# Performance work log

Hardware: AMD Instinct MI355X
Metric: run time of the kernel (lower is better)

The kernel has to match this reference:

```python
import jax, jax.numpy as jnp
import numpy as np

ACTIONS = 64
EMB = 32
DELTA = 16
EPS = 1e-5


def setup_inputs() -> dict:
    key = jax.random.key(0)
    k1, k2 = jax.random.split(key)
    n = 16384
    x = jax.random.normal(k1, (n, ACTIONS), dtype=jnp.float32)
    bn_weight = jnp.ones((ACTIONS,), dtype=jnp.float32)
    bn_bias = jnp.zeros((ACTIONS,), dtype=jnp.float32)
    emb_table = jax.random.normal(k2, ((2 * DELTA + 1) * ACTIONS, EMB), dtype=jnp.float32)
    return {"x": x, "bn_weight": bn_weight, "bn_bias": bn_bias, "emb_table": emb_table}


def reference(x, bn_weight, bn_bias, emb_table):
    n = x.shape[0]
    # BatchNorm1d in training mode: biased batch statistics over the batch dim
    mean = jnp.mean(x, axis=0)
    var = jnp.mean(jnp.square(x - mean), axis=0)
    xn = (x - mean) * jax.lax.rsqrt(var + EPS) * bn_weight + bn_bias
    t = jnp.clip(jnp.tanh(xn), -1.0 + 1e-5, 1.0 - 1e-5)  # [n, actions]

    ind_offset = jnp.arange(ACTIONS, dtype=jnp.int32)[None, :]  # [1, actions]
    xl = jnp.floor(t * DELTA)
    xli = ACTIONS * (xl.astype(jnp.int32) + DELTA) + ind_offset  # [n, actions]
    xl = xl / DELTA
    xh = jnp.floor(t * DELTA + 1.0)
    xhi = ACTIONS * (xh.astype(jnp.int32) + DELTA) + ind_offset
    xh = xh / DELTA

    bl = emb_table[xli]  # [n, actions, emb]
    bh = emb_table[xhi]  # [n, actions, emb]

    # h = bh/delta_inv*(t-xl) + bl/delta_inv*(xh-t), delta_inv = 1/DELTA
    t3 = t[..., None]
    h = bh * (DELTA * (t3 - xl[..., None])) + bl * (DELTA * (xh[..., None] - t3))
    return h
```

## Files before the change

### kernel.cpp

```cpp
#include <hip/hip_runtime.h>
#include <hip/hip_bf16.h>

#define ACTIONS 64
#define EMB 32
#define DELTA 16
#define EPS 1e-5f

typedef float f32x4 __attribute__((ext_vector_type(4)));

__device__ __forceinline__ float fast_tanhf(float x) {
    float e = __expf(2.0f * x);
    float r = __builtin_amdgcn_rcpf(1.0f + e);
    return 1.0f - 2.0f * r;
}

__global__ void __launch_bounds__(512) bn_stats_kernel(const f32x4* __restrict__ x4,
                                                       float* __restrict__ partial,
                                                       int total4 ) {
    const int tid = threadIdx.x;
    f32x4 s = {0.f, 0.f, 0.f, 0.f};
    f32x4 q = {0.f, 0.f, 0.f, 0.f};
    const int stride = gridDim.x * 512;
    for (int i = blockIdx.x * 512 + tid; i < total4; i += stride) {
        f32x4 v = x4[i];
        s += v;
        q += v * v;
    }
    __shared__ f32x4 ssum[512];
    __shared__ f32x4 ssq[512];
    ssum[tid] = s;
    ssq[tid] = q;
    __syncthreads();
    if (tid < 16) {
        f32x4 a = ssum[tid];
        f32x4 b = ssq[tid];
        #pragma unroll
        for (int k = 1; k < 32; ++k) {
            a += ssum[tid + 16 * k];
            b += ssq[tid + 16 * k];
        }
        float* ps = partial + blockIdx.x * 128;
        #pragma unroll
        for (int j = 0; j < 4; ++j) {
            ps[4 * tid + j]      = a[j];
            ps[64 + 4 * tid + j] = b[j];
        }
    }
}

__global__ void __launch_bounds__(256) spline_main_kernel(
        const f32x4* __restrict__ x4,
        const f32x4* __restrict__ emb4,
        const float* __restrict__ partial,
        const float* __restrict__ bn_w,
        const float* __restrict__ bn_b,
        f32x4* __restrict__ out4,
        float inv_n) {
    __shared__ f32x4 tab4[33 * 64];
    __shared__ f32x4 xs4[256];
    __shared__ float psum[2][8][16];

    const int tid     = threadIdx.x;
    const int colgrp  = blockIdx.x & 7;
    const int rowtile = blockIdx.x >> 3;
    const int c0      = colgrp * 8;
    const int r0      = rowtile * 128;

    for (int u = tid; u < 33 * 64; u += 256) {
        const int k = u >> 6, rest = u & 63;
        tab4[u] = emb4[k * 512 + c0 * 8 + rest];
    }
    xs4[tid] = x4[(r0 + (tid >> 1)) * 16 + (c0 >> 2) + (tid & 1)];

    {
        const int pci = tid & 7, half = (tid >> 3) & 1, chunk = tid >> 4;
        float s = 0.f;
        #pragma unroll
        for (int k = 0; k < 8; ++k)
            s += partial[(chunk * 8 + k) * 128 + half * 64 + c0 + pci];
        psum[half][pci][chunk] = s;
    }
    __syncthreads();

    const int ci      = (tid >> 3) & 7;
    const int e4      = tid & 7;
    const int row_off = tid >> 6;
    float scale, shift;
    {
        float s = 0.f, q = 0.f;
        #pragma unroll
        for (int k = 0; k < 16; ++k) { s += psum[0][ci][k]; q += psum[1][ci][k]; }
        const float mean = s * inv_n;
        const float var  = fmaxf(q * inv_n - mean * mean, 0.0f);
        scale = rsqrtf(var + EPS) * bn_w[c0 + ci];
        shift = bn_b[c0 + ci] - mean * scale;
    }

    const float* xs = (const float*)xs4;
    #pragma unroll 4
    for (int it = 0; it < 32; ++it) {
        const int rl = it * 4 + row_off;
        const float xv = xs[rl * 8 + ci];

        float t = fast_tanhf(fmaf(xv, scale, shift));
        t = fminf(fmaxf(t, -1.0f + 1e-5f), 1.0f - 1e-5f);

        const float td  = t * (float)DELTA;
        const float xlf = floorf(td);
        const float xhf = floorf(td + 1.0f);
        const int kl = (int)xlf + DELTA;
        const int kh = (int)xhf + DELTA;
        const float wl = xhf - td;
        const float wh = td - xlf;

        const f32x4 bl = tab4[kl * 64 + ci * 8 + e4];
        const f32x4 bh = tab4[kh * 64 + ci * 8 + e4];
        f32x4 o = bh * wh + bl * wl;
        out4[((r0 + rl) * ACTIONS + c0 + ci) * 8 + e4] = o;
    }
}

extern "C" void kernel_launch(void* const* d_in, const int* in_sizes, int n_in,
                              void* d_out, int out_size, void* d_ws, size_t ws_size,
                              hipStream_t stream) {
    const float* x    = (const float*)d_in[0];
    const float* bn_w = (const float*)d_in[1];
    const float* bn_b = (const float*)d_in[2];
    const float* emb  = (const float*)d_in[3];
    float* out        = (float*)d_out;

    const int n = in_sizes[0] / ACTIONS;
    const int total = n * ACTIONS;

    float* partial = (float*)d_ws;

    const int STATS_BLOCKS = 128;
    bn_stats_kernel<<<STATS_BLOCKS, 512, 0, stream>>>((const f32x4*)x, partial, total / 4);

    const int blocks = 8 * (n / 128);
    spline_main_kernel<<<blocks, 256, 0, stream>>>((const f32x4*)x, (const f32x4*)emb,
                                                   partial, bn_w, bn_b, (f32x4*)out,
                                                   1.0f / (float)n);
}
```

Before: 36.80 us.

## Fuse batch-stat reduction into spline kernel via cooperative grid sync

Removes the separate BN statistics kernel. Each spline block now computes per-column partial sums and sums of squares from the x tile it already loads into shared memory, writes them to workspace, and waits at a cooperative grid-wide barrier. After the barrier it reduces all partials to get mean and variance. This avoids a second launch and a second read of x, but requires all 1024 blocks to be co-resident and adds the cost of a grid barrier. Output stores are also switched to nontemporal stores, so the large output write does not pollute the caches.

```diff
diff --git a/kernel.cpp b/kernel.cpp
--- a/kernel.cpp
+++ b/kernel.cpp
@@ -1,5 +1,6 @@
 #include <hip/hip_runtime.h>
 #include <hip/hip_bf16.h>
+#include <hip/hip_cooperative_groups.h>
 
 #define ACTIONS 64
 #define EMB 32
@@ -14,51 +15,19 @@
     return 1.0f - 2.0f * r;
 }
 
-__global__ void __launch_bounds__(512) bn_stats_kernel(const f32x4* __restrict__ x4,
-                                                       float* __restrict__ partial,
-                                                       int total4 ) {
-    const int tid = threadIdx.x;
-    f32x4 s = {0.f, 0.f, 0.f, 0.f};
-    f32x4 q = {0.f, 0.f, 0.f, 0.f};
-    const int stride = gridDim.x * 512;
-    for (int i = blockIdx.x * 512 + tid; i < total4; i += stride) {
-        f32x4 v = x4[i];
-        s += v;
-        q += v * v;
-    }
-    __shared__ f32x4 ssum[512];
-    __shared__ f32x4 ssq[512];
-    ssum[tid] = s;
-    ssq[tid] = q;
-    __syncthreads();
-    if (tid < 16) {
-        f32x4 a = ssum[tid];
-        f32x4 b = ssq[tid];
-        #pragma unroll
-        for (int k = 1; k < 32; ++k) {
-            a += ssum[tid + 16 * k];
-            b += ssq[tid + 16 * k];
-        }
-        float* ps = partial + blockIdx.x * 128;
-        #pragma unroll
-        for (int j = 0; j < 4; ++j) {
-            ps[4 * tid + j]      = a[j];
-            ps[64 + 4 * tid + j] = b[j];
-        }
-    }
-}
-
-__global__ void __launch_bounds__(256) spline_main_kernel(
+__global__ void __launch_bounds__(256) spline_fused_kernel(
         const f32x4* __restrict__ x4,
         const f32x4* __restrict__ emb4,
-        const float* __restrict__ partial,
+        float* __restrict__ sums,
+        float* __restrict__ sqs,
         const float* __restrict__ bn_w,
         const float* __restrict__ bn_b,
         f32x4* __restrict__ out4,
-        float inv_n) {
+        float inv_n, int nrt ) {
     __shared__ f32x4 tab4[33 * 64];
     __shared__ f32x4 xs4[256];
-    __shared__ float psum[2][8][16];
+    __shared__ float scrA[32][8];
+    __shared__ float scrB[32][8];
 
     const int tid     = threadIdx.x;
     const int colgrp  = blockIdx.x & 7;
@@ -66,19 +35,46 @@
     const int c0      = colgrp * 8;
     const int r0      = rowtile * 128;
 
+    xs4[tid] = x4[(r0 + (tid >> 1)) * 16 + (c0 >> 2) + (tid & 1)];
     for (int u = tid; u < 33 * 64; u += 256) {
-        const int k = u >> 6, rest = u & 63;
-        tab4[u] = emb4[k * 512 + c0 * 8 + rest];
+        tab4[u] = emb4[(u >> 6) * 512 + c0 * 8 + (u & 63)];
     }
-    xs4[tid] = x4[(r0 + (tid >> 1)) * 16 + (c0 >> 2) + (tid & 1)];
+    __syncthreads();
+
+    const float* xs = (const float*)xs4;
+    {
+        const int ci = tid & 7, seg = tid >> 3;
+        float s = 0.f, q = 0.f;
+        #pragma unroll
+        for (int j = 0; j < 4; ++j) {
+            const float v = xs[(seg * 4 + j) * 8 + ci];
+            s += v;
+            q = fmaf(v, v, q);
+        }
+        scrA[seg][ci] = s;
+        scrB[seg][ci] = q;
+    }
+    __syncthreads();
+    if (tid < 8) {
+        float a = 0.f, b = 0.f;
+        #pragma unroll
+        for (int k = 0; k < 32; ++k) { a += scrA[k][tid]; b += scrB[k][tid]; }
+        sums[rowtile * 64 + c0 + tid] = a;
+        sqs [rowtile * 64 + c0 + tid] = b;
+    }
+
+    cooperative_groups::this_grid().sync();
 
     {
-        const int pci = tid & 7, half = (tid >> 3) & 1, chunk = tid >> 4;
-        float s = 0.f;
-        #pragma unroll
-        for (int k = 0; k < 8; ++k)
-            s += partial[(chunk * 8 + k) * 128 + half * 64 + c0 + pci];
-        psum[half][pci][chunk] = s;
+        const int ci = tid & 7, chunk = tid >> 3;
+        float s = 0.f, q = 0.f;
+        for (int j = 0; j < nrt; ++j) {
+            const int rt = chunk * nrt + j;
+            s += sums[rt * 64 + c0 + ci];
+            q += sqs [rt * 64 + c0 + ci];
+        }
+        scrA[chunk][ci] = s;
+        scrB[chunk][ci] = q;
     }
     __syncthreads();
 
@@ -87,16 +83,15 @@
     const int row_off = tid >> 6;
     float scale, shift;
     {
-        float s = 0.f, q = 0.f;
+        float S = 0.f, Q = 0.f;
         #pragma unroll
-        for (int k = 0; k < 16; ++k) { s += psum[0][ci][k]; q += psum[1][ci][k]; }
-        const float mean = s * inv_n;
-        const float var  = fmaxf(q * inv_n - mean * mean, 0.0f);
+        for (int k = 0; k < 32; ++k) { S += scrA[k][ci]; Q += scrB[k][ci]; }
+        const float mean = S * inv_n;
+        const float var  = fmaxf(Q * inv_n - mean * mean, 0.0f);
         scale = rsqrtf(var + EPS) * bn_w[c0 + ci];
         shift = bn_b[c0 + ci] - mean * scale;
     }
 
-    const float* xs = (const float*)xs4;
     #pragma unroll 4
     for (int it = 0; it < 32; ++it) {
         const int rl = it * 4 + row_off;
@@ -116,29 +111,32 @@
         const f32x4 bl = tab4[kl * 64 + ci * 8 + e4];
         const f32x4 bh = tab4[kh * 64 + ci * 8 + e4];
         f32x4 o = bh * wh + bl * wl;
-        out4[((r0 + rl) * ACTIONS + c0 + ci) * 8 + e4] = o;
+        __builtin_nontemporal_store(o, &out4[((r0 + rl) * ACTIONS + c0 + ci) * 8 + e4]);
     }
 }
 
 extern "C" void kernel_launch(void* const* d_in, const int* in_sizes, int n_in,
                               void* d_out, int out_size, void* d_ws, size_t ws_size,
                               hipStream_t stream) {
-    const float* x    = (const float*)d_in[0];
+    const f32x4* x4   = (const f32x4*)d_in[0];
     const float* bn_w = (const float*)d_in[1];
     const float* bn_b = (const float*)d_in[2];
-    const float* emb  = (const float*)d_in[3];
-    float* out        = (float*)d_out;
+    const f32x4* emb4 = (const f32x4*)d_in[3];
+    f32x4* out4       = (f32x4*)d_out;
 
     const int n = in_sizes[0] / ACTIONS;
-    const int total = n * ACTIONS;
+    const int nrowtiles = n / 128;
+    const int blocks = 8 * nrowtiles;
 
-    float* partial = (float*)d_ws;
+    float* sums = (float*)d_ws;
+    float* sqs  = (float*)d_ws + nrowtiles * 64;
 
-    const int STATS_BLOCKS = 128;
-    bn_stats_kernel<<<STATS_BLOCKS, 512, 0, stream>>>((const f32x4*)x, partial, total / 4);
+    float inv_n = 1.0f / (float)n;
+    int   nrt   = nrowtiles / 32;
 
-    const int blocks = 8 * (n / 128);
-    spline_main_kernel<<<blocks, 256, 0, stream>>>((const f32x4*)x, (const f32x4*)emb,
-                                                   partial, bn_w, bn_b, (f32x4*)out,
-                                                   1.0f / (float)n);
+    void* args[] = { (void*)&x4, (void*)&emb4, (void*)&sums, (void*)&sqs,
+                     (void*)&bn_w, (void*)&bn_b, (void*)&out4,
+                     (void*)&inv_n, (void*)&nrt };
+    hipLaunchCooperativeKernel((const void*)spline_fused_kernel,
+                               dim3(blocks), dim3(256), args, 0, stream);
 }
```

Result: slower. 82.24 us (+123.5%).
